# Kernel tuning notes

Measured on AMD Instinct MI355X. Metric: run time of the kernel, lower is better.

Reference implementation:

```python
import jax, jax.numpy as jnp
import numpy as np
from jax import lax

NX, NY = 6, 6
NB = NX * NY            # 36 blocks
B, S = 64, 256          # batch, sample_count
EPS = 1e-6

def build_edges(nx, ny):
    edges = []
    for i in range(nx):
        for j in range(ny):
            for dx, dy in [(-1, 0), (0, -1), (0, 1), (1, 0)]:
                x, y = i + dx, j + dy
                if 0 <= x < nx and 0 <= y < ny:
                    edges.append((j * nx + i, y * nx + x))
    return np.array(edges, np.int32)   # (120, 2)

EDGES_NP = build_edges(NX, NY)
NE = len(EDGES_NP)  # 120

def setup_inputs() -> dict:
    key = jax.random.key(0)
    ks = jax.random.split(key, 24)
    f32 = jnp.float32
    d = {
        "image":      jax.random.normal(ks[0], (B, 1, 32, 32), f32),
        "edge_noise": jax.random.uniform(ks[1], (B, S, NE), f32),
        "u_s":        jax.random.uniform(ks[2], (B, S, NB), f32),
        "u_d":        jax.random.uniform(ks[3], (B, S, NB), f32),
        # CNN params (OIHW)
        "cw1": jax.random.normal(ks[4], (32, 1, 5, 5), f32) * 0.05,
        "cb1": jnp.zeros((32,), f32),
        "cw2": jax.random.normal(ks[5], (32, 32, 5, 5), f32) * 0.05,
        "cb2": jnp.zeros((32,), f32),
        "cw3": jax.random.normal(ks[6], (64, 32, 5, 5), f32) * 0.05,
        "cb3": jnp.zeros((64,), f32),
        "cw4": jax.random.normal(ks[7], (64, 64, 5, 5), f32) * 0.05,
        "cb4": jnp.zeros((64,), f32),
        # is_connected MLP
        "wc1": jax.random.normal(ks[8], (256, 256), f32) * 0.05,
        "bc1": jnp.zeros((256,), f32),
        "wc2": jax.random.normal(ks[9], (256, NE), f32) * 0.05,
        "bc2": jnp.zeros((NE,), f32),
        # is_endpoint MLP
        "we1": jax.random.normal(ks[10], (256, 256), f32) * 0.05,
        "be1": jnp.zeros((256,), f32),
        "we2": jax.random.normal(ks[11], (256, NB), f32) * 0.05,
        "be2": jnp.zeros((NB,), f32),
        "edges": jnp.asarray(EDGES_NP),  # (NE, 2) int32, constants
    }
    return d

def _conv(x, w, b):
    y = lax.conv_general_dilated(x, w, (1, 1), 'VALID',
                                 dimension_numbers=('NCHW', 'OIHW', 'NCHW'))
    return y + b[None, :, None, None]

def _pool2(x):
    return lax.reduce_window(x, -jnp.inf, lax.max, (1, 1, 2, 2), (1, 1, 2, 2), 'VALID')

def reference(image, edge_noise, u_s, u_d,
              cw1, cb1, cw2, cb2, cw3, cb3, cw4, cb4,
              wc1, bc1, wc2, bc2, we1, be1, we2, be2, edges):
    # ---- CNN feature extractor ----
    h = _conv(image, cw1, cb1)
    h = _conv(h, cw2, cb2)
    h = _pool2(h)
    h = _conv(h, cw3, cb3)
    h = _conv(h, cw4, cb4)
    h = _pool2(h)
    emb = h.reshape(h.shape[0], -1)              # (B, 256)

    # ---- heads ----
    p_conn = jax.nn.sigmoid(jax.nn.relu(emb @ wc1 + bc1) @ wc2 + bc2)   # (B, NE)
    p_ep   = jax.nn.sigmoid(jax.nn.relu(emb @ we1 + be1) @ we2 + be2)   # (B, NB)

    pc = jnp.clip(p_conn, EPS, 1.0 - EPS)
    pe = jnp.clip(p_ep, EPS, 1.0 - EPS)
    cat = pe / pe.sum(-1, keepdims=True)
    logcat = jnp.log(cat)                        # (B, NB)

    # ---- Monte-Carlo sampling (ISED blackbox) ----
    conn = (edge_noise < pc[:, None, :]).astype(pc.dtype)               # (B,S,NE) Bernoulli
    g_s = -jnp.log(-jnp.log(jnp.clip(u_s, EPS, 1.0 - EPS)))
    g_d = -jnp.log(-jnp.log(jnp.clip(u_d, EPS, 1.0 - EPS)))
    s_idx = jnp.argmax(logcat[:, None, :] + g_s, axis=-1)               # (B,S) categorical
    d_idx = jnp.argmax(logcat[:, None, :] + g_d, axis=-1)               # (B,S)

    # ---- batched BFS reachability via boolean matrix squaring ----
    oh_u = jax.nn.one_hot(edges[:, 0], NB, dtype=pc.dtype)              # (NE, NB)
    oh_v = jax.nn.one_hot(edges[:, 1], NB, dtype=pc.dtype)
    e_sym = jnp.einsum('eu,ev->euv', oh_u, oh_v) + jnp.einsum('eu,ev->evu', oh_u, oh_v)
    A = jnp.minimum(jnp.einsum('bse,euv->bsuv', conn, e_sym), 1.0)      # (B,S,36,36)

    R = jnp.minimum(A + jnp.eye(NB, dtype=A.dtype), 1.0)
    for _ in range(6):                           # (I+A)^(2^6), covers path len<=36
        R = jnp.minimum(R @ R, 1.0)
    P = jnp.minimum(A @ R, 1.0)                  # paths of length >= 1 (BFS semantics)

    Pv = jnp.take_along_axis(P, s_idx[:, :, None, None], axis=2)[:, :, 0, :]  # (B,S,36)
    exists = (jnp.take_along_axis(Pv, d_idx[:, :, None], axis=2)[:, :, 0] > 0.5).astype(pc.dtype)  # (B,S)

    # ---- sample-probability weighting (differentiable ISED estimator) ----
    logw = (conn * jnp.log(pc)[:, None, :] + (1.0 - conn) * jnp.log1p(-pc)[:, None, :]).sum(-1)
    logw = logw + jnp.take_along_axis(logcat, s_idx, axis=1) \
                + jnp.take_along_axis(logcat, d_idx, axis=1)            # (B,S)
    w = jax.nn.softmax(logw, axis=1)
    p1 = (w * exists).sum(axis=1)                # P(path exists)
    return jnp.stack([1.0 - p1, p1], axis=-1)    # (B, 2)
```

## Files before the change

### kernel.cpp

```cpp
#include <hip/hip_runtime.h>

typedef unsigned long long u64;
#define EPSF 1e-6f

__global__ __launch_bounds__(512) void k_conv1(const float* __restrict__ img,
                                               const float* __restrict__ cw1,
                                               const float* __restrict__ cb1,
                                               float* __restrict__ c1) {
  int slab = blockIdx.x, b = blockIdx.y;
  __shared__ float simg[32 * 33];
  for (int k = threadIdx.x; k < 1024; k += 512) {
    int y = k >> 5, x = k & 31;
    simg[y * 33 + x] = img[b * 1024 + k];
  }
  int half = threadIdx.x >> 8;
  int u = threadIdx.x & 255;
  int ocl = u >> 5;
  int x = u & 31;
  int oc = slab * 8 + ocl;
  int y0 = half * 14;
  float w[25];
#pragma unroll
  for (int k = 0; k < 25; ++k) w[k] = cw1[oc * 25 + k];
  float bias = cb1[oc];
  __syncthreads();
  if (x < 28) {
    float acc[5];
#pragma unroll
    for (int k = 0; k < 5; ++k) acc[k] = bias;
    float* outp = c1 + (b * 32 + oc) * 784 + x;
#pragma unroll
    for (int rr = 0; rr < 18; ++rr) {
      int r = y0 + rr;
      float in[5];
#pragma unroll
      for (int c = 0; c < 5; ++c) in[c] = simg[r * 33 + x + c];
#pragma unroll
      for (int ky = 0; ky < 5; ++ky) {
        if (rr < ky || rr - ky > 13) continue;
        int slot = (rr - ky) % 5;
#pragma unroll
        for (int kx = 0; kx < 5; ++kx)
          acc[slot] = fmaf(w[ky * 5 + kx], in[kx], acc[slot]);
      }
      if (rr >= 4) {
        int slot = (rr - 4) % 5;
        outp[(y0 + rr - 4) * 28] = acc[slot];
        acc[slot] = bias;
      }
    }
  }
}

__global__ __launch_bounds__(512) void k_conv2(const float* __restrict__ c1,
                                               const float* __restrict__ cw2,
                                               const float* __restrict__ cb2,
                                               float* __restrict__ p1w) {
  int ocq = blockIdx.x, b = blockIdx.y;
  __shared__ float smem[29696];
  float* sInp = smem;
  float* pb = smem + 25088;
  int t = threadIdx.x;
  {
    const float4* src = (const float4*)(c1 + (size_t)b * 32 * 784);
    float4* dst = (float4*)sInp;
    for (int k = t; k < 6272; k += 512) dst[k] = src[k];
  }
  int w = __builtin_amdgcn_readfirstlane(t >> 6);
  int l = t & 63;
  int py = l >> 3, px = l & 7;
  int oc = ocq * 8 + w;
  const float* wrow = cw2 + (size_t)oc * 800;
  float acc[3][3];
#pragma unroll
  for (int i = 0; i < 3; ++i)
#pragma unroll
    for (int j = 0; j < 3; ++j) acc[i][j] = 0.f;
  __syncthreads();

  const float* base0 = sInp + 3 * py * 28 + 3 * px;
  for (int ic = 0; ic < 32; ++ic) {
    float w25[25];
    const float* wr = wrow + ic * 25;
#pragma unroll
    for (int k = 0; k < 25; ++k) w25[k] = wr[k];
    const float* base = base0 + ic * 784;
#pragma unroll
    for (int rr = 0; rr < 7; ++rr) {
      float win[7];
#pragma unroll
      for (int m = 0; m < 7; ++m) win[m] = base[rr * 28 + m];
#pragma unroll
      for (int i = 0; i < 3; ++i) {
        if (i > rr || rr - i > 4) continue;
        int ky = rr - i;
#pragma unroll
        for (int kx = 0; kx < 5; ++kx) {
#pragma unroll
          for (int j = 0; j < 3; ++j)
            acc[i][j] = fmaf(w25[ky * 5 + kx], win[j + kx], acc[i][j]);
        }
      }
    }
  }
  float bias = cb2[oc];
  float* pbw = pb + w * 576 + 3 * py * 24 + 3 * px;
#pragma unroll
  for (int i = 0; i < 3; ++i)
#pragma unroll
    for (int j = 0; j < 3; ++j) pbw[i * 24 + j] = acc[i][j] + bias;
  __syncthreads();
  for (int k = t; k < 1152; k += 512) {
    int o = k / 144, rem = k % 144;
    int PY = rem / 12, PX = rem % 12;
    const float* b0 = pb + o * 576 + (2 * PY) * 24 + 2 * PX;
    float m = fmaxf(fmaxf(b0[0], b0[1]), fmaxf(b0[24], b0[25]));
    p1w[((size_t)b * 32 + ocq * 8 + o) * 144 + PY * 12 + PX] = m;
  }
}

__global__ __launch_bounds__(256) void k_conv3(const float* __restrict__ p1w,
                                               const float* __restrict__ cw3,
                                               const float* __restrict__ cb3,
                                               float* __restrict__ c3) {
  int oc8 = blockIdx.x, b = blockIdx.y;
  __shared__ float smem[11008];
  float* w3s = smem;
  float* ins = smem + 6400;
  int t = threadIdx.x;
  {
    const float4* src = (const float4*)(p1w + b * 32 * 144);
    float4* dst = (float4*)ins;
    for (int k = t; k < 1152; k += 256) dst[k] = src[k];
  }
  {
    const float4* src = (const float4*)(cw3 + oc8 * 8 * 800);
    for (int k4 = t; k4 < 1600; k4 += 256) {
      float4 v = src[k4];
      float vv[4] = {v.x, v.y, v.z, v.w};
      int k = k4 * 4;
#pragma unroll
      for (int r = 0; r < 4; ++r) {
        int kk = k + r;
        int o = kk / 800, rest = kk % 800;
        w3s[rest * 8 + o] = vv[r];
      }
    }
  }
  int g = t >> 4, p = t & 15;
  int ocg = p >> 3, row = p & 7;
  float acc[4][8];
#pragma unroll
  for (int j = 0; j < 4; ++j)
#pragma unroll
    for (int c = 0; c < 8; ++c) acc[j][c] = 0.f;
  __syncthreads();
#pragma unroll
  for (int icl = 0; icl < 2; ++icl) {
    int ic = g + icl * 16;
#pragma unroll
    for (int ky = 0; ky < 5; ++ky) {
      const float4* rp = (const float4*)(ins + ic * 144 + (row + ky) * 12);
      float win[12];
#pragma unroll
      for (int q = 0; q < 3; ++q) {
        float4 v = rp[q];
        win[4 * q] = v.x; win[4 * q + 1] = v.y; win[4 * q + 2] = v.z; win[4 * q + 3] = v.w;
      }
      const float* wb = w3s + (ic * 25 + ky * 5) * 8 + ocg * 4;
#pragma unroll
      for (int kx = 0; kx < 5; ++kx) {
        float wq[4];
        *(float4*)wq = *(const float4*)(wb + kx * 8);
#pragma unroll
        for (int c = 0; c < 8; ++c) {
#pragma unroll
          for (int j = 0; j < 4; ++j) acc[j][c] = fmaf(wq[j], win[c + kx], acc[j][c]);
        }
      }
    }
  }
  float* buf = smem;
  __syncthreads();
  if (g >= 8) {
    float* d = buf + (g - 8) * 512 + p * 32;
#pragma unroll
    for (int j = 0; j < 4; ++j)
#pragma unroll
      for (int c = 0; c < 8; ++c) d[j * 8 + c] = acc[j][c];
  }
  __syncthreads();
  if (g < 8) {
    const float* s = buf + g * 512 + p * 32;
#pragma unroll
    for (int j = 0; j < 4; ++j)
#pragma unroll
      for (int c = 0; c < 8; ++c) acc[j][c] += s[j * 8 + c];
  }
  __syncthreads();
  if (g >= 4 && g < 8) {
    float* d = buf + (g - 4) * 512 + p * 32;
#pragma unroll
    for (int j = 0; j < 4; ++j)
#pragma unroll
      for (int c = 0; c < 8; ++c) d[j * 8 + c] = acc[j][c];
  }
  __syncthreads();
  if (g < 4) {
    const float* s = buf + g * 512 + p * 32;
#pragma unroll
    for (int j = 0; j < 4; ++j)
#pragma unroll
      for (int c = 0; c < 8; ++c) acc[j][c] += s[j * 8 + c];
  }
  __syncthreads();
  if (g == 2 || g == 3) {
    float* d = buf + (g - 2) * 512 + p * 32;
#pragma unroll
    for (int j = 0; j < 4; ++j)
#pragma unroll
      for (int c = 0; c < 8; ++c) d[j * 8 + c] = acc[j][c];
  }
  __syncthreads();
  if (g < 2) {
    const float* s = buf + g * 512 + p * 32;
#pragma unroll
    for (int j = 0; j < 4; ++j)
#pragma unroll
      for (int c = 0; c < 8; ++c) acc[j][c] += s[j * 8 + c];
  }
  __syncthreads();
  if (g == 1) {
    float* d = buf + p * 32;
#pragma unroll
    for (int j = 0; j < 4; ++j)
#pragma unroll
      for (int c = 0; c < 8; ++c) d[j * 8 + c] = acc[j][c];
  }
  __syncthreads();
  if (g == 0) {
    const float* s = buf + p * 32;
#pragma unroll
    for (int j = 0; j < 4; ++j) {
      float bias = cb3[oc8 * 8 + ocg * 4 + j];
      float4 v0, v1;
      v0.x = acc[j][0] + s[j * 8 + 0] + bias; v0.y = acc[j][1] + s[j * 8 + 1] + bias;
      v0.z = acc[j][2] + s[j * 8 + 2] + bias; v0.w = acc[j][3] + s[j * 8 + 3] + bias;
      v1.x = acc[j][4] + s[j * 8 + 4] + bias; v1.y = acc[j][5] + s[j * 8 + 5] + bias;
      v1.z = acc[j][6] + s[j * 8 + 6] + bias; v1.w = acc[j][7] + s[j * 8 + 7] + bias;
      float* op = c3 + (b * 64 + oc8 * 8 + ocg * 4 + j) * 64 + row * 8;
      *(float4*)op = v0; *(float4*)(op + 4) = v1;
    }
  }
}

__global__ __launch_bounds__(256) void k_conv4(const float* __restrict__ c3,
                                               const float* __restrict__ cw4,
                                               const float* __restrict__ cb4,
                                               float* __restrict__ emb) {
  int oc8 = blockIdx.x, b = blockIdx.y;
  __shared__ float smem[17152];
  float* w4s = smem;
  float* ins = smem + 12800;
  int t = threadIdx.x;
  {
    const float4* src = (const float4*)(c3 + b * 4096);
    for (int k = t; k < 1024; k += 256) {
      int ic = k >> 4, q = k & 15;
      *(float4*)(ins + ic * 68 + q * 4) = src[k];
    }
  }
  {
    const float4* src = (const float4*)(cw4 + oc8 * 8 * 1600);
    for (int k4 = t; k4 < 3200; k4 += 256) {
      float4 v = src[k4];
      float vv[4] = {v.x, v.y, v.z, v.w};
      int k = k4 * 4;
#pragma unroll
      for (int r = 0; r < 4; ++r) {
        int kk = k + r;
        int o = kk / 1600, rest = kk % 1600;
        w4s[rest * 8 + o] = vv[r];
      }
    }
  }
  int g = t >> 3, p = t & 7;
  int ocg = p >> 2, row = p & 3;
  float acc[4][4];
#pragma unroll
  for (int j = 0; j < 4; ++j)
#pragma unroll
    for (int c = 0; c < 4; ++c) acc[j][c] = 0.f;
  __syncthreads();
#pragma unroll
  for (int icl = 0; icl < 2; ++icl) {
    int ic = g + icl * 32;
#pragma unroll
    for (int ky = 0; ky < 5; ++ky) {
      const float4* rp = (const float4*)(ins + ic * 68 + (row + ky) * 8);
      float win[8];
#pragma unroll
      for (int q = 0; q < 2; ++q) {
        float4 v = rp[q];
        win[4 * q] = v.x; win[4 * q + 1] = v.y; win[4 * q + 2] = v.z; win[4 * q + 3] = v.w;
      }
      const float* wb = w4s + (ic * 25 + ky * 5) * 8 + ocg * 4;
#pragma unroll
      for (int kx = 0; kx < 5; ++kx) {
        float wq[4];
        *(float4*)wq = *(const float4*)(wb + kx * 8);
#pragma unroll
        for (int c = 0; c < 4; ++c) {
#pragma unroll
          for (int j = 0; j < 4; ++j) acc[j][c] = fmaf(wq[j], win[c + kx], acc[j][c]);
        }
      }
    }
  }
  float* buf = smem;
#pragma unroll
  for (int half = 16; half >= 1; half >>= 1) {
    __syncthreads();
    if (g >= half && g < 2 * half) {
      float* d = buf + (g - half) * 128 + p * 16;
#pragma unroll
      for (int j = 0; j < 4; ++j)
#pragma unroll
        for (int c = 0; c < 4; ++c) d[j * 4 + c] = acc[j][c];
    }
    __syncthreads();
    if (g < half) {
      const float* s = buf + g * 128 + p * 16;
#pragma unroll
      for (int j = 0; j < 4; ++j)
#pragma unroll
        for (int c = 0; c < 4; ++c) acc[j][c] += s[j * 4 + c];
    }
  }
  float* pb = buf + 2048;
  if (g == 0) {
#pragma unroll
    for (int j = 0; j < 4; ++j) {
      float bias = cb4[oc8 * 8 + ocg * 4 + j];
#pragma unroll
      for (int c = 0; c < 4; ++c) pb[(ocg * 4 + j) * 16 + row * 4 + c] = acc[j][c] + bias;
    }
  }
  __syncthreads();
  if (t < 32) {
    int o = t >> 2, q = t & 3, py = q >> 1, px = q & 1;
    const float* b0 = pb + o * 16 + (2 * py) * 4 + 2 * px;
    float m = fmaxf(fmaxf(b0[0], b0[1]), fmaxf(b0[4], b0[5]));
    emb[b * 256 + (oc8 * 8 + o) * 4 + py * 2 + px] = m;
  }
}

__global__ __launch_bounds__(256) void k_heads(const float* __restrict__ emb,
    const float* __restrict__ wc1, const float* __restrict__ bc1,
    const float* __restrict__ wc2, const float* __restrict__ bc2,
    const float* __restrict__ we1, const float* __restrict__ be1,
    const float* __restrict__ we2, const float* __restrict__ be2,
    float* __restrict__ pcw, float* __restrict__ lpcw,
    float* __restrict__ l1mw, float* __restrict__ lcatw) {
  int head = blockIdx.x, b = blockIdx.y;
  int t = threadIdx.x;
  __shared__ float e_s[256], h_s[256];
  __shared__ float aux;
  e_s[t] = emb[b * 256 + t];
  __syncthreads();
  const float* W1 = head ? we1 : wc1;
  const float* B1 = head ? be1 : bc1;
  float s = B1[t];
  for (int i = 0; i < 256; i += 4) {
    s = fmaf(e_s[i], W1[i * 256 + t], s);
    s = fmaf(e_s[i + 1], W1[(i + 1) * 256 + t], s);
    s = fmaf(e_s[i + 2], W1[(i + 2) * 256 + t], s);
    s = fmaf(e_s[i + 3], W1[(i + 3) * 256 + t], s);
  }
  h_s[t] = fmaxf(s, 0.f);
  __syncthreads();
  int NO = head ? 36 : 120;
  const float* W2 = head ? we2 : wc2;
  const float* B2 = head ? be2 : bc2;
  if (t < NO) {
    float s2 = B2[t];
    for (int i = 0; i < 256; ++i) s2 = fmaf(h_s[i], W2[i * NO + t], s2);
    float p = 1.f / (1.f + expf(-s2));
    p = fminf(fmaxf(p, EPSF), 1.f - EPSF);
    if (head == 0) {
      pcw[b * 120 + t] = p;
      lpcw[b * 120 + t] = logf(p);
      l1mw[b * 120 + t] = log1pf(-p);
    } else {
      e_s[t] = p;
    }
  }
  if (head == 1) {
    __syncthreads();
    if (t == 0) {
      float sm = 0.f;
      for (int j2 = 0; j2 < 36; ++j2) sm += e_s[j2];
      aux = sm;
    }
    __syncthreads();
    if (t < 36) lcatw[b * 36 + t] = logf(e_s[t] / aux);
  }
}

__global__ __launch_bounds__(256) void k_mc(const float* __restrict__ enoise,
    const float* __restrict__ us, const float* __restrict__ ud,
    const int* __restrict__ edges,
    const float* __restrict__ pcw, const float* __restrict__ lpcw,
    const float* __restrict__ l1mw, const float* __restrict__ lcatw,
    float* __restrict__ out) {
  int b = blockIdx.x, t = threadIdx.x;
  __shared__ __align__(16) float pc_s[120];
  __shared__ __align__(16) float lpc_s[120];
  __shared__ __align__(16) float l1m_s[120];
  __shared__ __align__(16) float lcat_s[36];
  __shared__ __align__(16) int einfo[120];
  __shared__ float red_s[256];
  if (t < 120) {
    pc_s[t] = pcw[b * 120 + t];
    lpc_s[t] = lpcw[b * 120 + t];
    l1m_s[t] = l1mw[b * 120 + t];
    int u = edges[2 * t], v = edges[2 * t + 1];
    int d = v - u;
    int isV = (d == 6 || d == -6) ? 1 : 0;
    int pos = d > 0 ? u : v;
    einfo[t] = pos | (isV << 6);
  }
  if (t < 36) lcat_s[t] = lcatw[b * 36 + t];
  __syncthreads();

  float logw = 0.f;
  u64 H = 0, V = 0;
  {
    const float4* np = (const float4*)(enoise + ((size_t)(b * 256 + t)) * 120);
#pragma unroll
    for (int q = 0; q < 30; ++q) {
      float4 nz = np[q];
      float4 p4 = ((const float4*)pc_s)[q];
      float4 lp4 = ((const float4*)lpc_s)[q];
      float4 lm4 = ((const float4*)l1m_s)[q];
      int4 e4 = ((const int4*)einfo)[q];
      float nv[4] = {nz.x, nz.y, nz.z, nz.w};
      float pv[4] = {p4.x, p4.y, p4.z, p4.w};
      float lv[4] = {lp4.x, lp4.y, lp4.z, lp4.w};
      float mv[4] = {lm4.x, lm4.y, lm4.z, lm4.w};
      int ev[4] = {e4.x, e4.y, e4.z, e4.w};
#pragma unroll
      for (int r = 0; r < 4; ++r) {
        bool conn = nv[r] < pv[r];
        logw += conn ? lv[r] : mv[r];
        if (conn) {
          u64 bit = 1ull << (ev[r] & 63);
          if (ev[r] & 64) V |= bit; else H |= bit;
        }
      }
    }
  }
  int si = 0, di = 0;
  {
    const float4* up = (const float4*)(us + ((size_t)(b * 256 + t)) * 36);
    float best = -1e30f;
#pragma unroll
    for (int q = 0; q < 9; ++q) {
      float4 uv = up[q];
      float4 lc4 = ((const float4*)lcat_s)[q];
      float vv[4] = {uv.x, uv.y, uv.z, uv.w};
      float lc[4] = {lc4.x, lc4.y, lc4.z, lc4.w};
#pragma unroll
      for (int r = 0; r < 4; ++r) {
        float u = fminf(fmaxf(vv[r], EPSF), 1.f - EPSF);
        float gq = -logf(-logf(u));
        float val = lc[r] + gq;
        if (val > best) { best = val; si = q * 4 + r; }
      }
    }
  }
  {
    const float4* up = (const float4*)(ud + ((size_t)(b * 256 + t)) * 36);
    float best = -1e30f;
#pragma unroll
    for (int q = 0; q < 9; ++q) {
      float4 uv = up[q];
      float4 lc4 = ((const float4*)lcat_s)[q];
      float vv[4] = {uv.x, uv.y, uv.z, uv.w};
      float lc[4] = {lc4.x, lc4.y, lc4.z, lc4.w};
#pragma unroll
      for (int r = 0; r < 4; ++r) {
        float u = fminf(fmaxf(vv[r], EPSF), 1.f - EPSF);
        float gq = -logf(-logf(u));
        float val = lc[r] + gq;
        if (val > best) { best = val; di = q * 4 + r; }
      }
    }
  }
  logw += lcat_s[si] + lcat_s[di];

  u64 comp = 1ull << si;
  while (true) {
    u64 prev = comp;
    comp |= ((comp & H) << 1) | ((comp >> 1) & H);
    comp |= ((comp & V) << 6) | ((comp >> 6) & V);
    if (comp == prev) break;
  }
  float ex;
  if (si == di) ex = (comp != (1ull << si)) ? 1.f : 0.f;
  else ex = ((comp >> di) & 1ull) ? 1.f : 0.f;

  red_s[t] = logw; __syncthreads();
  for (int off = 128; off > 0; off >>= 1) {
    if (t < off) red_s[t] = fmaxf(red_s[t], red_s[t + off]);
    __syncthreads();
  }
  float m = red_s[0]; __syncthreads();
  float evx = expf(logw - m);
  red_s[t] = evx; __syncthreads();
  for (int off = 128; off > 0; off >>= 1) {
    if (t < off) red_s[t] += red_s[t + off];
    __syncthreads();
  }
  float den = red_s[0]; __syncthreads();
  red_s[t] = evx * ex; __syncthreads();
  for (int off = 128; off > 0; off >>= 1) {
    if (t < off) red_s[t] += red_s[t + off];
    __syncthreads();
  }
  if (t == 0) {
    float p1v = red_s[0] / den;
    out[b * 2] = 1.f - p1v;
    out[b * 2 + 1] = p1v;
  }
}

extern "C" void kernel_launch(void* const* d_in, const int* in_sizes, int n_in,
                              void* d_out, int out_size, void* d_ws, size_t ws_size,
                              hipStream_t stream) {
  const float* image = (const float*)d_in[0];
  const float* enoise = (const float*)d_in[1];
  const float* us = (const float*)d_in[2];
  const float* udn = (const float*)d_in[3];
  const float* cw1 = (const float*)d_in[4];
  const float* cb1 = (const float*)d_in[5];
  const float* cw2 = (const float*)d_in[6];
  const float* cb2 = (const float*)d_in[7];
  const float* cw3 = (const float*)d_in[8];
  const float* cb3 = (const float*)d_in[9];
  const float* cw4 = (const float*)d_in[10];
  const float* cb4 = (const float*)d_in[11];
  const float* wc1 = (const float*)d_in[12];
  const float* bc1 = (const float*)d_in[13];
  const float* wc2 = (const float*)d_in[14];
  const float* bc2 = (const float*)d_in[15];
  const float* we1 = (const float*)d_in[16];
  const float* be1 = (const float*)d_in[17];
  const float* we2 = (const float*)d_in[18];
  const float* be2 = (const float*)d_in[19];
  const int* edges = (const int*)d_in[20];

  float* ws = (float*)d_ws;
  float* c1 = ws;
  float* p1w = ws + 1605632;
  float* c3 = ws + 1900544;
  float* emb = ws + 2162688;
  float* pcw = ws + 2179072;
  float* lpcw = ws + 2186752;
  float* l1mw = ws + 2194432;
  float* lcatw = ws + 2202112;
  float* outp = (float*)d_out;

  k_conv1<<<dim3(4, 64), dim3(512), 0, stream>>>(image, cw1, cb1, c1);
  k_conv2<<<dim3(4, 64), dim3(512), 0, stream>>>(c1, cw2, cb2, p1w);
  k_conv3<<<dim3(8, 64), dim3(256), 0, stream>>>(p1w, cw3, cb3, c3);
  k_conv4<<<dim3(8, 64), dim3(256), 0, stream>>>(c3, cw4, cb4, emb);
  k_heads<<<dim3(2, 64), dim3(256), 0, stream>>>(emb, wc1, bc1, wc2, bc2,
                                                 we1, be1, we2, be2,
                                                 pcw, lpcw, l1mw, lcatw);
  k_mc<<<dim3(64), dim3(256), 0, stream>>>(enoise, us, udn, edges,
                                           pcw, lpcw, l1mw, lcatw, outp);
}
```

Baseline: 127.0 us.

## Split conv2 input channels across two wave groups with shared-memory reduction

Doubles conv2 block size to 1024 threads, with each half of the waves handling 16 of the 32 input channels, then reduces the partial sums through shared memory before bias and max-pooling. The unrolled channel loop double-buffers weight registers so the next channel's weights load while the current channel computes. The aim is more waves in flight per output to hide LDS latency in conv2. The cost is an extra reduction pass, more barriers, and possibly higher register pressure at 1024 threads per block.

```diff
diff --git a/kernel.cpp b/kernel.cpp
--- a/kernel.cpp
+++ b/kernel.cpp
@@ -52,25 +52,26 @@
   }
 }
 
-__global__ __launch_bounds__(512) void k_conv2(const float* __restrict__ c1,
-                                               const float* __restrict__ cw2,
-                                               const float* __restrict__ cb2,
-                                               float* __restrict__ p1w) {
+__global__ __launch_bounds__(1024) void k_conv2(const float* __restrict__ c1,
+                                                const float* __restrict__ cw2,
+                                                const float* __restrict__ cb2,
+                                                float* __restrict__ p1w) {
   int ocq = blockIdx.x, b = blockIdx.y;
-  __shared__ float smem[29696];
+  __shared__ float smem[25088];
   float* sInp = smem;
-  float* pb = smem + 25088;
   int t = threadIdx.x;
   {
     const float4* src = (const float4*)(c1 + (size_t)b * 32 * 784);
     float4* dst = (float4*)sInp;
-    for (int k = t; k < 6272; k += 512) dst[k] = src[k];
+    for (int k = t; k < 6272; k += 1024) dst[k] = src[k];
   }
   int w = __builtin_amdgcn_readfirstlane(t >> 6);
+  int ocl = w & 7;
+  int ich = w >> 3;
   int l = t & 63;
   int py = l >> 3, px = l & 7;
-  int oc = ocq * 8 + w;
-  const float* wrow = cw2 + (size_t)oc * 800;
+  int oc = ocq * 8 + ocl;
+  const float* wrow = cw2 + (size_t)oc * 800 + ich * 16 * 25;
   float acc[3][3];
 #pragma unroll
   for (int i = 0; i < 3; ++i)
@@ -78,42 +79,67 @@
     for (int j = 0; j < 3; ++j) acc[i][j] = 0.f;
   __syncthreads();
 
-  const float* base0 = sInp + 3 * py * 28 + 3 * px;
-  for (int ic = 0; ic < 32; ++ic) {
-    float w25[25];
-    const float* wr = wrow + ic * 25;
-#pragma unroll
-    for (int k = 0; k < 25; ++k) w25[k] = wr[k];
-    const float* base = base0 + ic * 784;
-#pragma unroll
-    for (int rr = 0; rr < 7; ++rr) {
-      float win[7];
-#pragma unroll
-      for (int m = 0; m < 7; ++m) win[m] = base[rr * 28 + m];
-#pragma unroll
-      for (int i = 0; i < 3; ++i) {
-        if (i > rr || rr - i > 4) continue;
-        int ky = rr - i;
-#pragma unroll
-        for (int kx = 0; kx < 5; ++kx) {
-#pragma unroll
-          for (int j = 0; j < 3; ++j)
-            acc[i][j] = fmaf(w25[ky * 5 + kx], win[j + kx], acc[i][j]);
-        }
-      }
-    }
-  }
-  float bias = cb2[oc];
-  float* pbw = pb + w * 576 + 3 * py * 24 + 3 * px;
-#pragma unroll
-  for (int i = 0; i < 3; ++i)
-#pragma unroll
-    for (int j = 0; j < 3; ++j) pbw[i * 24 + j] = acc[i][j] + bias;
-  __syncthreads();
-  for (int k = t; k < 1152; k += 512) {
+  const float* base0 = sInp + (size_t)ich * 16 * 784 + 3 * py * 28 + 3 * px;
+
+  float wA[25], wB[25];
+#pragma unroll
+  for (int k = 0; k < 25; ++k) wA[k] = wrow[k];
+
+#define CONV2_IC(ICL, WREG)                                                  \
+  {                                                                          \
+    const float* base = base0 + (ICL) * 784;                                 \
+    _Pragma("unroll") for (int rr = 0; rr < 7; ++rr) {                       \
+      float win[7];                                                          \
+      _Pragma("unroll") for (int m = 0; m < 7; ++m) win[m] = base[rr * 28 + m]; \
+      _Pragma("unroll") for (int i = 0; i < 3; ++i) {                        \
+        if (i > rr || rr - i > 4) continue;                                  \
+        int ky = rr - i;                                                     \
+        _Pragma("unroll") for (int kx = 0; kx < 5; ++kx) {                   \
+          _Pragma("unroll") for (int j = 0; j < 3; ++j)                      \
+            acc[i][j] = fmaf(WREG[ky * 5 + kx], win[j + kx], acc[i][j]);     \
+        }                                                                    \
+      }                                                                      \
+    }                                                                        \
+  }
+
+#pragma unroll
+  for (int icp = 0; icp < 8; ++icp) {
+#pragma unroll
+    for (int k = 0; k < 25; ++k) wB[k] = wrow[(2 * icp + 1) * 25 + k];
+    CONV2_IC(2 * icp, wA)
+    if (icp < 7) {
+#pragma unroll
+      for (int k = 0; k < 25; ++k) wA[k] = wrow[(2 * icp + 2) * 25 + k];
+    }
+    CONV2_IC(2 * icp + 1, wB)
+  }
+#undef CONV2_IC
+
+  __syncthreads();
+  float* red = smem;
+  float* cb = smem + 4608;
+  if (ich == 1) {
+    float* d = red + ocl * 576 + 3 * py * 24 + 3 * px;
+#pragma unroll
+    for (int i = 0; i < 3; ++i)
+#pragma unroll
+      for (int j = 0; j < 3; ++j) d[i * 24 + j] = acc[i][j];
+  }
+  __syncthreads();
+  if (ich == 0) {
+    float bias = cb2[oc];
+    const float* s = red + ocl * 576 + 3 * py * 24 + 3 * px;
+    float* d = cb + ocl * 576 + 3 * py * 24 + 3 * px;
+#pragma unroll
+    for (int i = 0; i < 3; ++i)
+#pragma unroll
+      for (int j = 0; j < 3; ++j) d[i * 24 + j] = acc[i][j] + s[i * 24 + j] + bias;
+  }
+  __syncthreads();
+  for (int k = t; k < 1152; k += 1024) {
     int o = k / 144, rem = k % 144;
     int PY = rem / 12, PX = rem % 12;
-    const float* b0 = pb + o * 576 + (2 * PY) * 24 + 2 * PX;
+    const float* b0 = cb + o * 576 + (2 * PY) * 24 + 2 * PX;
     float m = fmaxf(fmaxf(b0[0], b0[1]), fmaxf(b0[24], b0[25]));
     p1w[((size_t)b * 32 + ocq * 8 + o) * 144 + PY * 12 + PX] = m;
   }
@@ -572,7 +598,7 @@
   float* outp = (float*)d_out;
 
   k_conv1<<<dim3(4, 64), dim3(512), 0, stream>>>(image, cw1, cb1, c1);
-  k_conv2<<<dim3(4, 64), dim3(512), 0, stream>>>(c1, cw2, cb2, p1w);
+  k_conv2<<<dim3(4, 64), dim3(1024), 0, stream>>>(c1, cw2, cb2, p1w);
   k_conv3<<<dim3(8, 64), dim3(256), 0, stream>>>(p1w, cw3, cb3, c3);
   k_conv4<<<dim3(8, 64), dim3(256), 0, stream>>>(c3, cw4, cb4, emb);
   k_heads<<<dim3(2, 64), dim3(256), 0, stream>>>(emb, wc1, bc1, wc2, bc2,
```

New measurement: 126.9 us. Within noise of the previous version (-0.1%).

## Split conv2 input channels across 16 waves with shared-memory reduction

Applied to the files above, without the earlier changes.

The conv2 kernel now runs 1024 threads per block. Each wave computes two output channels over a quarter of the input channels, then partial sums are reduced through shared memory in a two-step tree. The input tile is also stored with a row pitch of 29 to reduce LDS bank conflicts. This raises parallelism per block and register-level reuse of input windows, at the cost of extra syncs, a reduction pass, and higher register pressure at 1024 threads.

```diff
diff --git a/kernel.cpp b/kernel.cpp
--- a/kernel.cpp
+++ b/kernel.cpp
@@ -52,44 +52,50 @@
   }
 }
 
-__global__ __launch_bounds__(512) void k_conv2(const float* __restrict__ c1,
-                                               const float* __restrict__ cw2,
-                                               const float* __restrict__ cb2,
-                                               float* __restrict__ p1w) {
+__global__ __launch_bounds__(1024) void k_conv2(const float* __restrict__ c1,
+                                                const float* __restrict__ cw2,
+                                                const float* __restrict__ cb2,
+                                                float* __restrict__ p1w) {
   int ocq = blockIdx.x, b = blockIdx.y;
-  __shared__ float smem[29696];
-  float* sInp = smem;
-  float* pb = smem + 25088;
+  __shared__ float smem[25984];
   int t = threadIdx.x;
   {
-    const float4* src = (const float4*)(c1 + (size_t)b * 32 * 784);
-    float4* dst = (float4*)sInp;
-    for (int k = t; k < 6272; k += 512) dst[k] = src[k];
+    const float4* src = (const float4*)(c1 + (size_t)b * 25088);
+    for (int k = t; k < 6272; k += 1024) {
+      float4 v = src[k];
+      int ic = k / 196, rem = k % 196;
+      int row = rem / 7, c4 = rem % 7;
+      float* d = smem + ic * 812 + row * 29 + c4 * 4;
+      d[0] = v.x; d[1] = v.y; d[2] = v.z; d[3] = v.w;
+    }
   }
   int w = __builtin_amdgcn_readfirstlane(t >> 6);
+  int opair = w & 3;
+  int icq = w >> 2;
   int l = t & 63;
   int py = l >> 3, px = l & 7;
-  int oc = ocq * 8 + w;
-  const float* wrow = cw2 + (size_t)oc * 800;
-  float acc[3][3];
-#pragma unroll
-  for (int i = 0; i < 3; ++i)
-#pragma unroll
-    for (int j = 0; j < 3; ++j) acc[i][j] = 0.f;
-  __syncthreads();
-
-  const float* base0 = sInp + 3 * py * 28 + 3 * px;
-  for (int ic = 0; ic < 32; ++ic) {
-    float w25[25];
-    const float* wr = wrow + ic * 25;
-#pragma unroll
-    for (int k = 0; k < 25; ++k) w25[k] = wr[k];
-    const float* base = base0 + ic * 784;
+  int oc0 = ocq * 8 + opair * 2;
+  const float* wApt = cw2 + (size_t)oc0 * 800 + icq * 200;
+  const float* wBpt = wApt + 800;
+  float acc[2][9];
+#pragma unroll
+  for (int j = 0; j < 2; ++j)
+#pragma unroll
+    for (int e = 0; e < 9; ++e) acc[j][e] = 0.f;
+  __syncthreads();
+
+  const float* base0 = smem + icq * 8 * 812 + (3 * py) * 29 + 3 * px;
+#pragma unroll
+  for (int ic = 0; ic < 8; ++ic) {
+    float wa[25], wb[25];
+#pragma unroll
+    for (int k = 0; k < 25; ++k) { wa[k] = wApt[ic * 25 + k]; wb[k] = wBpt[ic * 25 + k]; }
+    const float* base = base0 + ic * 812;
 #pragma unroll
     for (int rr = 0; rr < 7; ++rr) {
       float win[7];
 #pragma unroll
-      for (int m = 0; m < 7; ++m) win[m] = base[rr * 28 + m];
+      for (int m = 0; m < 7; ++m) win[m] = base[rr * 29 + m];
 #pragma unroll
       for (int i = 0; i < 3; ++i) {
         if (i > rr || rr - i > 4) continue;
@@ -97,23 +103,64 @@
 #pragma unroll
         for (int kx = 0; kx < 5; ++kx) {
 #pragma unroll
-          for (int j = 0; j < 3; ++j)
-            acc[i][j] = fmaf(w25[ky * 5 + kx], win[j + kx], acc[i][j]);
+          for (int jj = 0; jj < 3; ++jj) {
+            acc[0][i * 3 + jj] = fmaf(wa[ky * 5 + kx], win[jj + kx], acc[0][i * 3 + jj]);
+            acc[1][i * 3 + jj] = fmaf(wb[ky * 5 + kx], win[jj + kx], acc[1][i * 3 + jj]);
+          }
         }
       }
     }
   }
-  float bias = cb2[oc];
-  float* pbw = pb + w * 576 + 3 * py * 24 + 3 * px;
-#pragma unroll
-  for (int i = 0; i < 3; ++i)
-#pragma unroll
-    for (int j = 0; j < 3; ++j) pbw[i * 24 + j] = acc[i][j] + bias;
-  __syncthreads();
-  for (int k = t; k < 1152; k += 512) {
+
+  __syncthreads();
+  float* slot0 = smem;
+  float* slot1 = smem + 4608;
+  float* cbuf = smem + 9216;
+  if (icq >= 2) {
+    float* d = (icq == 2) ? slot0 : slot1;
+#pragma unroll
+    for (int j = 0; j < 2; ++j)
+#pragma unroll
+      for (int e = 0; e < 9; ++e) d[((opair * 2 + j) * 64 + l) * 9 + e] = acc[j][e];
+  }
+  __syncthreads();
+  if (icq == 0) {
+#pragma unroll
+    for (int j = 0; j < 2; ++j)
+#pragma unroll
+      for (int e = 0; e < 9; ++e) acc[j][e] += slot0[((opair * 2 + j) * 64 + l) * 9 + e];
+  }
+  if (icq == 1) {
+#pragma unroll
+    for (int j = 0; j < 2; ++j)
+#pragma unroll
+      for (int e = 0; e < 9; ++e) acc[j][e] += slot1[((opair * 2 + j) * 64 + l) * 9 + e];
+  }
+  __syncthreads();
+  if (icq == 1) {
+#pragma unroll
+    for (int j = 0; j < 2; ++j)
+#pragma unroll
+      for (int e = 0; e < 9; ++e) slot0[((opair * 2 + j) * 64 + l) * 9 + e] = acc[j][e];
+  }
+  __syncthreads();
+  if (icq == 0) {
+#pragma unroll
+    for (int j = 0; j < 2; ++j) {
+      float bias = cb2[oc0 + j];
+#pragma unroll
+      for (int i = 0; i < 3; ++i)
+#pragma unroll
+        for (int jj = 0; jj < 3; ++jj)
+          cbuf[(opair * 2 + j) * 576 + (3 * py + i) * 24 + 3 * px + jj] =
+              acc[j][i * 3 + jj] + slot0[((opair * 2 + j) * 64 + l) * 9 + i * 3 + jj] + bias;
+    }
+  }
+  __syncthreads();
+  for (int k = t; k < 1152; k += 1024) {
     int o = k / 144, rem = k % 144;
     int PY = rem / 12, PX = rem % 12;
-    const float* b0 = pb + o * 576 + (2 * PY) * 24 + 2 * PX;
+    const float* b0 = cbuf + o * 576 + (2 * PY) * 24 + 2 * PX;
     float m = fmaxf(fmaxf(b0[0], b0[1]), fmaxf(b0[24], b0[25]));
     p1w[((size_t)b * 32 + ocq * 8 + o) * 144 + PY * 12 + PX] = m;
   }
@@ -572,7 +619,7 @@
   float* outp = (float*)d_out;
 
   k_conv1<<<dim3(4, 64), dim3(512), 0, stream>>>(image, cw1, cb1, c1);
-  k_conv2<<<dim3(4, 64), dim3(512), 0, stream>>>(c1, cw2, cb2, p1w);
+  k_conv2<<<dim3(4, 64), dim3(1024), 0, stream>>>(c1, cw2, cb2, p1w);
   k_conv3<<<dim3(8, 64), dim3(256), 0, stream>>>(p1w, cw3, cb3, c3);
   k_conv4<<<dim3(8, 64), dim3(256), 0, stream>>>(c3, cw4, cb4, emb);
   k_heads<<<dim3(2, 64), dim3(256), 0, stream>>>(emb, wc1, bc1, wc2, bc2,
```

Result: faster. 118.7 us (-6.5%).
